# Kernel tuning notes

Hardware: AMD Instinct MI355X
Metric: run time of the kernel (lower is better)

## Reference

```python
import jax, jax.numpy as jnp
import numpy as np


def gaussian_window(window_size, stdev):
    w = window_size // 2
    x = jnp.linspace(-w, w, window_size)
    return jnp.exp(-(x[None, :] ** 2 + x[:, None] ** 2) / stdev ** 2)


def setup_inputs() -> dict:
    key = jax.random.key(0)
    B, A, K, H, W = 64, 8, 17, 256, 256
    WS, STDEV = 11, 3.0
    heatmap = jnp.zeros((B, K, H, W), dtype=jnp.float32)
    # keypoints[..., 0]=x, [...,1]=y, [...,2]=visibility (vis>=1 means labeled)
    keypoints = jax.random.randint(key, (B, A, K, 3), 0, 256, dtype=jnp.int32)
    window = gaussian_window(WS, STDEV).astype(jnp.float32)
    return {"heatmap": heatmap, "window": window, "keypoints": keypoints}


def reference(heatmap, window, keypoints):
    # heatmap: [B, K, H, W]; window: [WS, WS]; keypoints: [B, A, K, 3] int
    B, K, H, W = heatmap.shape
    WS = window.shape[0]
    hw = WS // 2
    xs = keypoints[..., 0]  # [B, A, K]
    ys = keypoints[..., 1]
    vis = keypoints[..., 2]
    off = jnp.arange(WS) - hw
    rows = ys[..., None] + off              # [B, A, K, WS]
    cols = xs[..., None] + off              # [B, A, K, WS]
    in_r = (rows >= 0) & (rows < H)
    in_c = (cols >= 0) & (cols < W)
    # mask: in-bounds window pixel AND keypoint visible
    mask = in_r[..., :, None] & in_c[..., None, :] & (vis >= 1)[..., None, None]
    vals = jnp.where(mask, window, -jnp.inf)  # [B, A, K, WS, WS]
    rows_c = jnp.clip(rows, 0, H - 1)[..., :, None]  # [B, A, K, WS, 1]
    cols_c = jnp.clip(cols, 0, W - 1)[..., None, :]  # [B, A, K, 1, WS]
    bi = jnp.arange(B)[:, None, None, None, None]
    ki = jnp.arange(K)[None, None, :, None, None]
    # scatter-max of all Gaussian windows into the heatmap (mode='max' of set_window)
    return heatmap.at[bi, ki, rows_c, cols_c].max(vals)
```

## Files before the change

### kernel.cpp

```cpp
#include <hip/hip_runtime.h>

#define NB 64
#define NA 8
#define NK 17
#define NH 256
#define NW 256
#define WS 11
#define HWIN 5

__global__ __launch_bounds__(256) void heatmap_gather_kernel(
    const float* __restrict__ window,
    const int*   __restrict__ keypoints,
    float*       __restrict__ out)
{
    __shared__ float win[WS * WS];
    __shared__ int kx[NA], ky[NA], kv[NA];

    const int plane = blockIdx.x;
    const int b = plane / NK;
    const int k = plane - b * NK;
    const int tid = threadIdx.x;

    if (tid < WS * WS) win[tid] = window[tid];
    if (tid < NA) {
        const int base = ((b * NA + tid) * NK + k) * 3;
        kx[tid] = keypoints[base + 0];
        ky[tid] = keypoints[base + 1];
        kv[tid] = keypoints[base + 2];
    }
    __syncthreads();

    const int row  = (blockIdx.y << 2) + (tid >> 6);
    const int lane = tid & 63;
    const int w0   = lane << 2;

    float acc0 = 0.f, acc1 = 0.f, acc2 = 0.f, acc3 = 0.f;

    #pragma unroll
    for (int a = 0; a < NA; ++a) {
        const int dy = row - ky[a];
        if (kv[a] >= 1 && dy >= -HWIN && dy <= HWIN) {
            const float* wrow = &win[(dy + HWIN) * WS];
            const int x = kx[a];
            int dx;
            dx = w0 + 0 - x; if (dx >= -HWIN && dx <= HWIN) acc0 = fmaxf(acc0, wrow[dx + HWIN]);
            dx = w0 + 1 - x; if (dx >= -HWIN && dx <= HWIN) acc1 = fmaxf(acc1, wrow[dx + HWIN]);
            dx = w0 + 2 - x; if (dx >= -HWIN && dx <= HWIN) acc2 = fmaxf(acc2, wrow[dx + HWIN]);
            dx = w0 + 3 - x; if (dx >= -HWIN && dx <= HWIN) acc3 = fmaxf(acc3, wrow[dx + HWIN]);
        }
    }

    const size_t idx = ((size_t)plane * NH + row) * NW + w0;
    *reinterpret_cast<float4*>(&out[idx]) = make_float4(acc0, acc1, acc2, acc3);
}

extern "C" void kernel_launch(void* const* d_in, const int* in_sizes, int n_in,
                              void* d_out, int out_size, void* d_ws, size_t ws_size,
                              hipStream_t stream) {
    const float* window    = (const float*)d_in[1];
    const int*   keypoints = (const int*)d_in[2];
    float*       out       = (float*)d_out;

    dim3 grid(NB * NK, NH / 4);
    heatmap_gather_kernel<<<grid, 256, 0, stream>>>(window, keypoints, out);
}
```

Measured before the change: 52.77 us.

## Compute four rows per wave and load keypoints directly into registers

Each wave now produces a 4x4 tile per lane (four rows) instead of one row, so grid.y shrinks by four. Keypoint data is read straight from global memory per thread (uniform, cached) rather than staged through shared memory. This amortizes block setup, window staging and keypoint loads over more output, at the cost of more registers and fewer blocks for a kernel that is bound by output writes.

```diff
diff --git a/kernel.cpp b/kernel.cpp
--- a/kernel.cpp
+++ b/kernel.cpp
@@ -14,44 +14,57 @@
     float*       __restrict__ out)
 {
     __shared__ float win[WS * WS];
-    __shared__ int kx[NA], ky[NA], kv[NA];
+    const int tid = threadIdx.x;
+    if (tid < WS * WS) win[tid] = window[tid];
 
     const int plane = blockIdx.x;
     const int b = plane / NK;
     const int k = plane - b * NK;
-    const int tid = threadIdx.x;
 
-    if (tid < WS * WS) win[tid] = window[tid];
-    if (tid < NA) {
-        const int base = ((b * NA + tid) * NK + k) * 3;
-        kx[tid] = keypoints[base + 0];
-        ky[tid] = keypoints[base + 1];
-        kv[tid] = keypoints[base + 2];
-    }
+    const int wave = tid >> 6;
+    const int lane = tid & 63;
+    const int row0 = (blockIdx.y << 4) + (wave << 2);
+    const int w0   = lane << 2;
+
     __syncthreads();
 
-    const int row  = (blockIdx.y << 2) + (tid >> 6);
-    const int lane = tid & 63;
-    const int w0   = lane << 2;
-
-    float acc0 = 0.f, acc1 = 0.f, acc2 = 0.f, acc3 = 0.f;
+    float acc[4][4];
+    #pragma unroll
+    for (int r = 0; r < 4; ++r)
+        #pragma unroll
+        for (int j = 0; j < 4; ++j) acc[r][j] = 0.f;
 
     #pragma unroll
     for (int a = 0; a < NA; ++a) {
-        const int dy = row - ky[a];
-        if (kv[a] >= 1 && dy >= -HWIN && dy <= HWIN) {
-            const float* wrow = &win[(dy + HWIN) * WS];
-            const int x = kx[a];
-            int dx;
-            dx = w0 + 0 - x; if (dx >= -HWIN && dx <= HWIN) acc0 = fmaxf(acc0, wrow[dx + HWIN]);
-            dx = w0 + 1 - x; if (dx >= -HWIN && dx <= HWIN) acc1 = fmaxf(acc1, wrow[dx + HWIN]);
-            dx = w0 + 2 - x; if (dx >= -HWIN && dx <= HWIN) acc2 = fmaxf(acc2, wrow[dx + HWIN]);
-            dx = w0 + 3 - x; if (dx >= -HWIN && dx <= HWIN) acc3 = fmaxf(acc3, wrow[dx + HWIN]);
+        const int base = ((b * NA + a) * NK + k) * 3;
+        const int x    = keypoints[base + 0];
+        const int y    = keypoints[base + 1];
+        const int vis  = keypoints[base + 2];
+        const int ky   = (vis >= 1) ? y : -1000;
+        const int dy0  = row0 - ky;
+        if ((unsigned)(dy0 + HWIN + 3) <= (unsigned)(2 * HWIN + 3)) {
+            #pragma unroll
+            for (int r = 0; r < 4; ++r) {
+                const int dy = dy0 + r;
+                if ((unsigned)(dy + HWIN) <= (unsigned)(2 * HWIN)) {
+                    const float* wrow = &win[(dy + HWIN) * WS];
+                    #pragma unroll
+                    for (int j = 0; j < 4; ++j) {
+                        const int dx = w0 + j - x;
+                        if ((unsigned)(dx + HWIN) <= (unsigned)(2 * HWIN))
+                            acc[r][j] = fmaxf(acc[r][j], wrow[dx + HWIN]);
+                    }
+                }
+            }
         }
     }
 
-    const size_t idx = ((size_t)plane * NH + row) * NW + w0;
-    *reinterpret_cast<float4*>(&out[idx]) = make_float4(acc0, acc1, acc2, acc3);
+    const size_t rowbase = ((size_t)plane * NH + row0) * NW + w0;
+    #pragma unroll
+    for (int r = 0; r < 4; ++r) {
+        *reinterpret_cast<float4*>(&out[rowbase + (size_t)r * NW]) =
+            make_float4(acc[r][0], acc[r][1], acc[r][2], acc[r][3]);
+    }
 }
 
 extern "C" void kernel_launch(void* const* d_in, const int* in_sizes, int n_in,
@@ -61,6 +74,6 @@
     const int*   keypoints = (const int*)d_in[2];
     float*       out       = (float*)d_out;
 
-    dim3 grid(NB * NK, NH / 4);
+    dim3 grid(NB * NK, NH / 16);
     heatmap_gather_kernel<<<grid, 256, 0, stream>>>(window, keypoints, out);
 }
```

After: 44.21 us. 1.19x faster.
